# Kernel optimization log

Measured on AMD Instinct MI355X. Metric: run time of the kernel, lower is better.

The kernel has to match this reference:

```python
import jax, jax.numpy as jnp
import numpy as np
from jax import lax

NUM_HEADS = 8
HEAD_SIZE = 256  # hidden_size // num_heads

def _layernorm(x, g, b, eps=1e-5):
    mu = jnp.mean(x, axis=-1, keepdims=True)
    var = jnp.mean((x - mu) ** 2, axis=-1, keepdims=True)
    return (x - mu) * lax.rsqrt(var + eps) * g + b

def _groupnorm(x, g, b, num_groups, eps=1e-5):
    B, C = x.shape
    xr = x.reshape(B, num_groups, C // num_groups)
    mu = jnp.mean(xr, axis=-1, keepdims=True)
    var = jnp.mean((xr - mu) ** 2, axis=-1, keepdims=True)
    xn = ((xr - mu) * lax.rsqrt(var + eps)).reshape(B, C)
    return xn * g + b

def _block_diag(x, W, b):
    # x: (B, nb*fi), W: (nb, fi, fo), b: (nb, fo) -> (B, nb*fo)
    B = x.shape[0]
    nb, fi, fo = W.shape
    y = jnp.einsum('bnf,nfo->bno', x.reshape(B, nb, fi), W) + b
    return y.reshape(B, nb * fo)

def _causal_conv1d(x, w, b):
    # x: (B, L); w: (1,1,4). Pad-both-sides-3 then drop last 3 == left-pad 3.
    y = lax.conv_general_dilated(x[:, None, :], w, (1,), [(3, 0)])
    return y[:, 0, :] + b

def _mlstm_forward(x, ln_g, ln_b, Wupl, bupl, Wupr, bupr, conv_w, conv_b,
                   Wskip, bskip, Wq, bq, Wk, bk, Wv, bv, Wi, bi, Wf, bf,
                   Wo, bo, gn_g, gn_b, Wdown, bdown, c_prev, n_prev, m_prev):
    x_norm = _layernorm(x, ln_g, ln_b)
    x_up_left = x_norm @ Wupl + bupl           # (B, 2D)
    x_up_right = x_norm @ Wupr + bupr          # (B, H)
    x_conv = jax.nn.silu(_causal_conv1d(x_up_left, conv_w, conv_b))
    x_skip = x_conv @ Wskip + bskip            # (B, H)
    q = _block_diag(x_conv, Wq, bq)
    k = _block_diag(x_conv, Wk, bk) / (HEAD_SIZE ** 0.5)
    v = _block_diag(x_up_left, Wv, bv)
    i_tilde = x_conv @ Wi + bi
    f_tilde = x_conv @ Wf + bf
    o = jax.nn.sigmoid(x_up_left @ Wo + bo)
    m_t = jnp.maximum(f_tilde + m_prev, i_tilde)
    i_g = jnp.exp(i_tilde - m_t)
    f_g = jnp.exp(f_tilde + m_prev - m_t)
    c_t = f_g * c_prev + i_g * (v * k)
    n_t = f_g * n_prev + i_g * k
    denom = jnp.max(jnp.abs(n_t.T @ q), axis=1)  # (H,) broadcast over batch
    h_t = o * (c_t * q) / denom
    out = _groupnorm(h_t, gn_g, gn_b, NUM_HEADS) + x_skip
    out = out * jax.nn.silu(x_up_right)
    final = out @ Wdown + bdown + x
    return (final, h_t, c_t, n_t, m_t)

def setup_inputs():
    key = jax.random.key(0)
    ks = jax.random.split(key, 16)
    B, D, H, NB = 8192, 1024, 2048, 8
    UP = 2 * D
    rnd = lambda k, shp, s=0.02: jax.random.normal(k, shp, jnp.float32) * s
    return {
        'x': jax.random.normal(ks[0], (B, D), jnp.float32),
        'ln_g': jnp.ones((D,), jnp.float32), 'ln_b': jnp.zeros((D,), jnp.float32),
        'Wupl': rnd(ks[1], (D, UP)), 'bupl': jnp.zeros((UP,), jnp.float32),
        'Wupr': rnd(ks[2], (D, H)), 'bupr': jnp.zeros((H,), jnp.float32),
        'conv_w': rnd(ks[3], (1, 1, 4), 0.3), 'conv_b': jnp.zeros((1,), jnp.float32),
        'Wskip': rnd(ks[4], (UP, H)), 'bskip': jnp.zeros((H,), jnp.float32),
        'Wq': rnd(ks[5], (NB, UP // NB, H // NB)), 'bq': jnp.zeros((NB, H // NB), jnp.float32),
        'Wk': rnd(ks[6], (NB, UP // NB, H // NB)), 'bk': jnp.zeros((NB, H // NB), jnp.float32),
        'Wv': rnd(ks[7], (NB, UP // NB, H // NB)), 'bv': jnp.zeros((NB, H // NB), jnp.float32),
        'Wi': rnd(ks[8], (UP, H)), 'bi': jnp.zeros((H,), jnp.float32),
        'Wf': rnd(ks[9], (UP, H)), 'bf': jnp.zeros((H,), jnp.float32),
        'Wo': rnd(ks[10], (UP, H)), 'bo': jnp.zeros((H,), jnp.float32),
        'gn_g': jnp.ones((H,), jnp.float32), 'gn_b': jnp.zeros((H,), jnp.float32),
        'Wdown': rnd(ks[11], (H, D)), 'bdown': jnp.zeros((D,), jnp.float32),
        'c_prev': rnd(ks[12], (B, H)), 'n_prev': jnp.ones((B, H), jnp.float32),
        'm_prev': jnp.zeros((B, H), jnp.float32),
    }

def reference(x, ln_g, ln_b, Wupl, bupl, Wupr, bupr, conv_w, conv_b, Wskip, bskip,
              Wq, bq, Wk, bk, Wv, bv, Wi, bi, Wf, bf, Wo, bo, gn_g, gn_b,
              Wdown, bdown, c_prev, n_prev, m_prev):
    return _mlstm_forward(x, ln_g, ln_b, Wupl, bupl, Wupr, bupr, conv_w, conv_b,
                          Wskip, bskip, Wq, bq, Wk, bk, Wv, bv, Wi, bi, Wf, bf,
                          Wo, bo, gn_g, gn_b, Wdown, bdown, c_prev, n_prev, m_prev)
```

## Files before the change

### kernel.cpp

```cpp
#include <hip/hip_runtime.h>


typedef __bf16 bf16_t;
typedef bf16_t bf16x8 __attribute__((ext_vector_type(8)));
typedef bf16_t bf16x4 __attribute__((ext_vector_type(4)));
typedef float f32x4 __attribute__((ext_vector_type(4)));

#define B_ROWS 8192
#define DMODEL 1024
#define HDIM   2048

__device__ __forceinline__ void gload_lds16(const void* g, void* s) {
  __builtin_amdgcn_global_load_lds(
      (const __attribute__((address_space(1))) void*)g,
      (__attribute__((address_space(3))) void*)s, 16, 0, 0);
}

__device__ __forceinline__ float sigmoidf_(float x) { return 1.f / (1.f + __expf(-x)); }
__device__ __forceinline__ float siluf_(float x)    { return x / (1.f + __expf(-x)); }

__device__ __forceinline__ int xcd_swz(int lin, int nwg) {
  const int q = nwg >> 3, r = nwg & 7;
  const int xcd = lin & 7, sub = lin >> 3;
  return (xcd < r ? xcd * (q + 1) : r * (q + 1) + (xcd - r) * q) + sub;
}

__global__ __launch_bounds__(256) void wtrans_kernel(
    const float* __restrict__ in, bf16_t* __restrict__ out, int R, int C) {
  const int z = blockIdx.z;
  in  += (size_t)z * R * C;
  out += (size_t)z * R * C;
  __shared__ float tile[64][65];
  const int t = threadIdx.x;
  const int r0 = blockIdx.y * 64, c0 = blockIdx.x * 64;
#pragma unroll
  for (int j = 0; j < 4; ++j) {
    const int r = j * 16 + (t >> 4);
    const int c = (t & 15) * 4;
    float4 v = *(const float4*)&in[(size_t)(r0 + r) * C + c0 + c];
    tile[r][c] = v.x; tile[r][c + 1] = v.y; tile[r][c + 2] = v.z; tile[r][c + 3] = v.w;
  }
  __syncthreads();
#pragma unroll
  for (int j = 0; j < 2; ++j) {
    const int wi = j * 256 + t;
    const int oc = wi >> 3;
    const int orr = (wi & 7) * 8;
    bf16x8 v;
#pragma unroll
    for (int u = 0; u < 8; ++u) v[u] = (bf16_t)tile[orr + u][oc];
    *(bf16x8*)&out[(size_t)(c0 + oc) * R + r0 + orr] = v;
  }
}

__global__ __launch_bounds__(256) void ln_kernel(
    const float* __restrict__ x, const float* __restrict__ g,
    const float* __restrict__ b, bf16_t* __restrict__ out) {
  const int row = blockIdx.x;
  const int t = threadIdx.x;
  const float* xr = x + (size_t)row * DMODEL;
  float4 v = *(const float4*)&xr[t * 4];
  float s = v.x + v.y + v.z + v.w;
  float s2 = v.x * v.x + v.y * v.y + v.z * v.z + v.w * v.w;
#pragma unroll
  for (int off = 1; off < 64; off <<= 1) {
    s += __shfl_xor(s, off, 64);
    s2 += __shfl_xor(s2, off, 64);
  }
  __shared__ float ps[8];
  const int w = t >> 6;
  if ((t & 63) == 0) { ps[w] = s; ps[4 + w] = s2; }
  __syncthreads();
  s = ps[0] + ps[1] + ps[2] + ps[3];
  s2 = ps[4] + ps[5] + ps[6] + ps[7];
  const float mu = s / (float)DMODEL;
  const float var = s2 / (float)DMODEL - mu * mu;
  const float rstd = rsqrtf(var + 1e-5f);
  float4 gg = *(const float4*)&g[t * 4];
  float4 bb = *(const float4*)&b[t * 4];
  bf16x4 o;
  o[0] = (bf16_t)((v.x - mu) * rstd * gg.x + bb.x);
  o[1] = (bf16_t)((v.y - mu) * rstd * gg.y + bb.y);
  o[2] = (bf16_t)((v.z - mu) * rstd * gg.z + bb.z);
  o[3] = (bf16_t)((v.w - mu) * rstd * gg.w + bb.w);
  *(bf16x4*)&out[(size_t)row * DMODEL + t * 4] = o;
}

__global__ __launch_bounds__(256) void conv_kernel(
    const bf16_t* __restrict__ xin, const float* __restrict__ cw,
    const float* __restrict__ cb, bf16_t* __restrict__ yb) {
  const size_t idx = (size_t)blockIdx.x * blockDim.x + threadIdx.x;
  const int row = (int)(idx >> 9);
  const int c0 = ((int)idx & 511) * 4;
  const bf16_t* xr = xin + (size_t)row * HDIM;
  const float w0 = cw[0], w1 = cw[1], w2 = cw[2], w3 = cw[3], bb = cb[0];
  float xm3 = 0.f, xm2 = 0.f, xm1 = 0.f;
  if (c0 > 0) {
    bf16x4 p = *(const bf16x4*)&xr[c0 - 4];
    xm3 = (float)p[1]; xm2 = (float)p[2]; xm1 = (float)p[3];
  }
  bf16x4 xv4 = *(const bf16x4*)&xr[c0];
  float x0 = (float)xv4[0], x1 = (float)xv4[1], x2 = (float)xv4[2], x3 = (float)xv4[3];
  float y0 = w0 * xm3 + w1 * xm2 + w2 * xm1 + w3 * x0 + bb;
  float y1 = w0 * xm2 + w1 * xm1 + w2 * x0 + w3 * x1 + bb;
  float y2 = w0 * xm1 + w1 * x0 + w2 * x1 + w3 * x2 + bb;
  float y3 = w0 * x0 + w1 * x1 + w2 * x2 + w3 * x3 + bb;
  bf16x4 yb4;
  yb4[0] = (bf16_t)siluf_(y0); yb4[1] = (bf16_t)siluf_(y1);
  yb4[2] = (bf16_t)siluf_(y2); yb4[3] = (bf16_t)siluf_(y3);
  *(bf16x4*)&yb[(size_t)row * HDIM + c0] = yb4;
}

__global__ __launch_bounds__(256) void hgn_kernel(
    const bf16_t* __restrict__ o_pre, const float* __restrict__ q,
    const float* __restrict__ c_t, const float* __restrict__ denomf,
    const bf16_t* __restrict__ skip, const bf16_t* __restrict__ upr,
    const float* __restrict__ gn_g, const float* __restrict__ gn_b,
    float* __restrict__ h_out, bf16_t* __restrict__ act_out) {
  const int row = blockIdx.x;
  const int t = threadIdx.x;
  const size_t base = (size_t)row * HDIM + t * 8;
  const int i0 = t * 8;
  bf16x8 o8 = *(const bf16x8*)&o_pre[base];
  float h[8];
  float s = 0.f, s2 = 0.f;
#pragma unroll
  for (int j = 0; j < 2; ++j) {
    float4 qv = *(const float4*)&q[base + j * 4];
    float4 cv = *(const float4*)&c_t[base + j * 4];
#pragma unroll
    for (int u = 0; u < 4; ++u) {
      const int k = j * 4 + u;
      float hv = sigmoidf_((float)o8[k]) * ((const float*)&cv)[u] *
                 ((const float*)&qv)[u] / denomf[i0 + k];
      h[k] = hv;
      s += hv;
      s2 += hv * hv;
    }
  }
#pragma unroll
  for (int off = 1; off < 32; off <<= 1) {
    s += __shfl_xor(s, off, 64);
    s2 += __shfl_xor(s2, off, 64);
  }
  const float mu = s / 256.f;
  const float var = s2 / 256.f - mu * mu;
  const float rstd = rsqrtf(var + 1e-5f);
  float4 h0 = {h[0], h[1], h[2], h[3]};
  float4 h1 = {h[4], h[5], h[6], h[7]};
  *(float4*)&h_out[base] = h0;
  *(float4*)&h_out[base + 4] = h1;
  bf16x8 sk8 = *(const bf16x8*)&skip[base];
  bf16x8 up8 = *(const bf16x8*)&upr[base];
  bf16x8 a8;
#pragma unroll
  for (int j = 0; j < 2; ++j) {
    float4 gv = *(const float4*)&gn_g[i0 + j * 4];
    float4 bv = *(const float4*)&gn_b[i0 + j * 4];
#pragma unroll
    for (int u = 0; u < 4; ++u) {
      const int k = j * 4 + u;
      float y = (h[k] - mu) * rstd * ((const float*)&gv)[u] + ((const float*)&bv)[u];
      y = (y + (float)sk8[k]) * siluf_((float)up8[k]);
      a8[k] = (bf16_t)y;
    }
  }
  *(bf16x8*)&act_out[base] = a8;
}

template <int OUTMODE, bool RES>
__global__ __launch_bounds__(256) void gemm_kernel(
    const bf16_t* __restrict__ A, int lda, const bf16_t* __restrict__ Bt, int ldb,
    const float* __restrict__ bias, float* __restrict__ C, bf16_t* __restrict__ Cb,
    int ldc, const float* __restrict__ res, int ldres, int K, float scale,
    int zA, long long zB, int zBias, int zC) {
  const int z = blockIdx.z;
  A += (size_t)z * zA;
  Bt += (size_t)z * zB;
  if (bias) bias += (size_t)z * zBias;
  if (OUTMODE == 0) C += (size_t)z * zC; else Cb += (size_t)z * zC;
  const int brow = blockIdx.y * 128;
  const int bcol = blockIdx.x * 128;
  __shared__ bf16_t As[128 * 32];
  __shared__ bf16_t Bs[128 * 32];
  const int tid = threadIdx.x;
  const int w = tid >> 6, l = tid & 63;
  const int wr = w >> 1, wc = w & 1;
  const int lr = l & 15, kg = l >> 4;
  const int l4 = l & 3, ld4 = l >> 2;

  f32x4 acc[4][4];
  const f32x4 fzero = {0.f, 0.f, 0.f, 0.f};
#pragma unroll
  for (int m = 0; m < 4; ++m)
#pragma unroll
    for (int n = 0; n < 4; ++n) acc[m][n] = fzero;

  for (int kt = 0; kt < K; kt += 32) {
#pragma unroll
    for (int j = 0; j < 2; ++j) {
      const int rowX = w * 32 + j * 16 + ld4;
      gload_lds16(A + (size_t)(brow + rowX) * lda + kt + l4 * 8, &As[w * 1024 + j * 512]);
      gload_lds16(Bt + (size_t)(bcol + rowX) * ldb + kt + l4 * 8, &Bs[w * 1024 + j * 512]);
    }
    __syncthreads();
    bf16x8 a[4], b[4];
#pragma unroll
    for (int m = 0; m < 4; ++m)
      a[m] = *(const bf16x8*)&As[(wr * 64 + m * 16 + lr) * 32 + kg * 8];
#pragma unroll
    for (int n = 0; n < 4; ++n)
      b[n] = *(const bf16x8*)&Bs[(wc * 64 + n * 16 + lr) * 32 + kg * 8];
#pragma unroll
    for (int m = 0; m < 4; ++m)
#pragma unroll
      for (int n = 0; n < 4; ++n)
        acc[m][n] = __builtin_amdgcn_mfma_f32_16x16x32_bf16(a[m], b[n], acc[m][n], 0, 0, 0);
    __syncthreads();
  }

#pragma unroll
  for (int m = 0; m < 4; ++m) {
    const int row0 = brow + wr * 64 + m * 16 + kg * 4;
#pragma unroll
    for (int n = 0; n < 4; ++n) {
      const int col = bcol + wc * 64 + n * 16 + lr;
      const float bv = bias ? bias[col] : 0.f;
#pragma unroll
      for (int r = 0; r < 4; ++r) {
        const int row = row0 + r;
        float v = (acc[m][n][r] + bv) * scale;
        if (RES) v += res[(size_t)row * ldres + col];
        if (OUTMODE == 0) C[(size_t)row * ldc + col] = v;
        else Cb[(size_t)row * ldc + col] = (bf16_t)v;
      }
    }
  }
}

template <int OUTMODE , bool RES>
__global__ __launch_bounds__(512, 2) void gemm256_kernel(
    const bf16_t* __restrict__ A, int lda, const bf16_t* __restrict__ Bt, int ldb,
    const float* __restrict__ bias, float* __restrict__ C, bf16_t* __restrict__ Cb,
    int ldc, const float* __restrict__ res, int ldres, int K, float scale,
    long long zA, long long zB, long long zC) {
  const int z = blockIdx.z;
  A += (size_t)z * zA;
  Bt += (size_t)z * zB;
  if (OUTMODE == 0) C += (size_t)z * zC; else Cb += (size_t)z * zC;

  const int nwg = gridDim.x * gridDim.y;
  const int lin2 = xcd_swz(blockIdx.y * gridDim.x + blockIdx.x, nwg);
  const int bx = lin2 % gridDim.x, by = lin2 / gridDim.x;
  const int brow = by * 256, bcol = bx * 256;

  __shared__ bf16_t As[2][256 * 64];
  __shared__ bf16_t Bs[2][256 * 64];

  const int tid = threadIdx.x;
  const int l = tid & 63;
  const int w = tid >> 6;
  const int wr = w >> 2, wn = w & 3;
  const int lr = l & 15, kg = l >> 4;
  const int srow = tid >> 3;
  const int sslot = (tid & 7) ^ (srow & 7);

  f32x4 acc[8][4];
  const f32x4 fzero = {0.f, 0.f, 0.f, 0.f};
#pragma unroll
  for (int m = 0; m < 8; ++m)
#pragma unroll
    for (int n = 0; n < 4; ++n) acc[m][n] = fzero;

  const int NT = K >> 6;
  const bf16_t* Ag = A + (size_t)brow * lda;
  const bf16_t* Bg = Bt + (size_t)bcol * ldb;

  auto stage = [&](int t, int buf) {
    const size_t kof = (size_t)t * 64 + sslot * 8;
#pragma unroll
    for (int j = 0; j < 4; ++j) {
      const int r = j * 64 + srow;
      gload_lds16(Ag + (size_t)r * lda + kof, (char*)&As[buf][0] + (j * 512 + tid) * 16);
      gload_lds16(Bg + (size_t)r * ldb + kof, (char*)&Bs[buf][0] + (j * 512 + tid) * 16);
    }
  };

  stage(0, 0);
  stage(1, 1);

  for (int t = 0; t < NT; ++t) {
    if (t < NT - 1) asm volatile("s_waitcnt vmcnt(8)" ::: "memory");
    else            asm volatile("s_waitcnt vmcnt(0)" ::: "memory");
    __builtin_amdgcn_s_barrier();
    const int buf = t & 1;
#pragma unroll
    for (int kk = 0; kk < 2; ++kk) {
      bf16x8 a[8], b[4];
#pragma unroll
      for (int n = 0; n < 4; ++n) {
        const int r = wn * 64 + n * 16 + lr;
        b[n] = *(const bf16x8*)&Bs[buf][r * 64 + (((kk * 4 + kg) ^ (r & 7)) * 8)];
      }
#pragma unroll
      for (int m = 0; m < 8; ++m) {
        const int r = wr * 128 + m * 16 + lr;
        a[m] = *(const bf16x8*)&As[buf][r * 64 + (((kk * 4 + kg) ^ (r & 7)) * 8)];
      }
      __builtin_amdgcn_s_setprio(1);
#pragma unroll
      for (int m = 0; m < 8; ++m)
#pragma unroll
        for (int n = 0; n < 4; ++n)
          acc[m][n] = __builtin_amdgcn_mfma_f32_16x16x32_bf16(a[m], b[n], acc[m][n], 0, 0, 0);
      __builtin_amdgcn_s_setprio(0);
    }
    asm volatile("s_waitcnt lgkmcnt(0)" ::: "memory");
    __builtin_amdgcn_sched_barrier(0);
    __builtin_amdgcn_s_barrier();
    if (t + 2 < NT) stage(t + 2, buf);
  }

#pragma unroll
  for (int m = 0; m < 8; ++m) {
    const int row0 = brow + wr * 128 + m * 16 + kg * 4;
#pragma unroll
    for (int n = 0; n < 4; ++n) {
      const int col = bcol + wn * 64 + n * 16 + lr;
      const float bvv = bias ? bias[col] : 0.f;
#pragma unroll
      for (int r = 0; r < 4; ++r) {
        const int row = row0 + r;
        float v = (acc[m][n][r] + bvv) * scale;
        if (RES) v += res[(size_t)row * ldres + col];
        if (OUTMODE == 0) C[(size_t)row * ldc + col] = v;
        else Cb[(size_t)row * ldc + col] = (bf16_t)v;
      }
    }
  }
}

__global__ __launch_bounds__(512, 2) void ifgate256_kernel(
    const bf16_t* __restrict__ A,
    const bf16_t* __restrict__ Bi, const bf16_t* __restrict__ Bf,
    const float* __restrict__ bi, const float* __restrict__ bfv,
    const float* __restrict__ m_prev, const float* __restrict__ c_prev,
    const float* __restrict__ n_prev,
    const bf16_t* __restrict__ vb, const bf16_t* __restrict__ kb,
    float* __restrict__ m_out, float* __restrict__ c_out, float* __restrict__ n_out) {
  const int nwg = gridDim.x * gridDim.y;
  const int lin2 = xcd_swz(blockIdx.y * gridDim.x + blockIdx.x, nwg);
  const int bx = lin2 % gridDim.x, by = lin2 / gridDim.x;
  const int brow = by * 256, bcol = bx * 128;

  __shared__ bf16_t As[2][256 * 64];
  __shared__ bf16_t Bis[2][128 * 64];
  __shared__ bf16_t Bfs[2][128 * 64];

  const int tid = threadIdx.x;
  const int l = tid & 63;
  const int w = tid >> 6;
  const int wr = w >> 2, wn = w & 3;
  const int lr = l & 15, kg = l >> 4;
  const int srow = tid >> 3;
  const int sslot = (tid & 7) ^ (srow & 7);

  f32x4 acci[8][2], accf[8][2];
  const f32x4 fzero = {0.f, 0.f, 0.f, 0.f};
#pragma unroll
  for (int m = 0; m < 8; ++m)
#pragma unroll
    for (int n = 0; n < 2; ++n) { acci[m][n] = fzero; accf[m][n] = fzero; }

  const int NT = HDIM >> 6;
  const bf16_t* Ag = A + (size_t)brow * HDIM;
  const bf16_t* Big = Bi + (size_t)bcol * HDIM;
  const bf16_t* Bfg = Bf + (size_t)bcol * HDIM;

  auto stage = [&](int t, int buf) {
    const size_t kof = (size_t)t * 64 + sslot * 8;
#pragma unroll
    for (int j = 0; j < 4; ++j) {
      const int r = j * 64 + srow;
      gload_lds16(Ag + (size_t)r * HDIM + kof, (char*)&As[buf][0] + (j * 512 + tid) * 16);
    }
#pragma unroll
    for (int j = 0; j < 2; ++j) {
      const int r = j * 64 + srow;
      gload_lds16(Big + (size_t)r * HDIM + kof, (char*)&Bis[buf][0] + (j * 512 + tid) * 16);
      gload_lds16(Bfg + (size_t)r * HDIM + kof, (char*)&Bfs[buf][0] + (j * 512 + tid) * 16);
    }
  };

  stage(0, 0);
  stage(1, 1);

  for (int t = 0; t < NT; ++t) {
    if (t < NT - 1) asm volatile("s_waitcnt vmcnt(8)" ::: "memory");
    else            asm volatile("s_waitcnt vmcnt(0)" ::: "memory");
    __builtin_amdgcn_s_barrier();
    const int buf = t & 1;
#pragma unroll
    for (int kk = 0; kk < 2; ++kk) {
      bf16x8 a[8], b1[2], b2[2];
#pragma unroll
      for (int n = 0; n < 2; ++n) {
        const int r = wn * 32 + n * 16 + lr;
        const int eo = r * 64 + (((kk * 4 + kg) ^ (r & 7)) * 8);
        b1[n] = *(const bf16x8*)&Bis[buf][eo];
        b2[n] = *(const bf16x8*)&Bfs[buf][eo];
      }
#pragma unroll
      for (int m = 0; m < 8; ++m) {
        const int r = wr * 128 + m * 16 + lr;
        a[m] = *(const bf16x8*)&As[buf][r * 64 + (((kk * 4 + kg) ^ (r & 7)) * 8)];
      }
      __builtin_amdgcn_s_setprio(1);
#pragma unroll
      for (int m = 0; m < 8; ++m)
#pragma unroll
        for (int n = 0; n < 2; ++n) {
          acci[m][n] = __builtin_amdgcn_mfma_f32_16x16x32_bf16(a[m], b1[n], acci[m][n], 0, 0, 0);
          accf[m][n] = __builtin_amdgcn_mfma_f32_16x16x32_bf16(a[m], b2[n], accf[m][n], 0, 0, 0);
        }
      __builtin_amdgcn_s_setprio(0);
    }
    asm volatile("s_waitcnt lgkmcnt(0)" ::: "memory");
    __builtin_amdgcn_sched_barrier(0);
    __builtin_amdgcn_s_barrier();
    if (t + 2 < NT) stage(t + 2, buf);
  }

#pragma unroll
  for (int m = 0; m < 8; ++m) {
    const int row0 = brow + wr * 128 + m * 16 + kg * 4;
#pragma unroll
    for (int n = 0; n < 2; ++n) {
      const int col = bcol + wn * 32 + n * 16 + lr;
      const float biv = bi[col], bfvv = bfv[col];
#pragma unroll
      for (int r = 0; r < 4; ++r) {
        const int row = row0 + r;
        const size_t idx = (size_t)row * HDIM + col;
        const float it = acci[m][n][r] + biv;
        const float ft = accf[m][n][r] + bfvv;
        const float m1 = m_prev[idx];
        const float mt = fmaxf(ft + m1, it);
        const float ig = __expf(it - mt);
        const float fg = __expf(ft + m1 - mt);
        const float v1 = (float)vb[idx], k1 = (float)kb[idx];
        m_out[idx] = mt;
        c_out[idx] = fg * c_prev[idx] + ig * (v1 * k1);
        n_out[idx] = fg * n_prev[idx] + ig * k1;
      }
    }
  }
}

__global__ __launch_bounds__(256) void denom_reduce_kernel(
    const float* __restrict__ part, float* __restrict__ dmaxf) {
  const int i = blockIdx.x;
  const int t = threadIdx.x;
  float vmax = 0.f;
#pragma unroll
  for (int u = 0; u < 8; ++u) {
    const int j = u * 256 + t;
    float s = 0.f;
#pragma unroll
    for (int zz = 0; zz < 4; ++zz)
      s += part[(size_t)zz * HDIM * HDIM + (size_t)i * HDIM + j];
    vmax = fmaxf(vmax, fabsf(s));
  }
#pragma unroll
  for (int off = 1; off < 64; off <<= 1) vmax = fmaxf(vmax, __shfl_xor(vmax, off, 64));
  __shared__ float ps[4];
  if ((t & 63) == 0) ps[t >> 6] = vmax;
  __syncthreads();
  if (t == 0) dmaxf[i] = fmaxf(fmaxf(ps[0], ps[1]), fmaxf(ps[2], ps[3]));
}

extern "C" void kernel_launch(void* const* d_in, const int* in_sizes, int n_in,
                              void* d_out, int out_size, void* d_ws, size_t ws_size,
                              hipStream_t stream) {
  (void)in_sizes; (void)n_in; (void)out_size; (void)ws_size;
  const float* x      = (const float*)d_in[0];
  const float* ln_g   = (const float*)d_in[1];
  const float* ln_b   = (const float*)d_in[2];
  const float* Wupl   = (const float*)d_in[3];
  const float* bupl   = (const float*)d_in[4];
  const float* Wupr   = (const float*)d_in[5];
  const float* bupr   = (const float*)d_in[6];
  const float* conv_w = (const float*)d_in[7];
  const float* conv_b = (const float*)d_in[8];
  const float* Wskip  = (const float*)d_in[9];
  const float* bskip  = (const float*)d_in[10];
  const float* Wq     = (const float*)d_in[11];
  const float* bq     = (const float*)d_in[12];
  const float* Wk     = (const float*)d_in[13];
  const float* bk     = (const float*)d_in[14];
  const float* Wv     = (const float*)d_in[15];
  const float* bv     = (const float*)d_in[16];
  const float* Wi     = (const float*)d_in[17];
  const float* bi     = (const float*)d_in[18];
  const float* Wf     = (const float*)d_in[19];
  const float* bf_    = (const float*)d_in[20];
  const float* Wo     = (const float*)d_in[21];
  const float* bo     = (const float*)d_in[22];
  const float* gn_g   = (const float*)d_in[23];
  const float* gn_b   = (const float*)d_in[24];
  const float* Wdown  = (const float*)d_in[25];
  const float* bdown  = (const float*)d_in[26];
  const float* c_prev = (const float*)d_in[27];
  const float* n_prev = (const float*)d_in[28];
  const float* m_prev = (const float*)d_in[29];

  float* out_final = (float*)d_out;
  float* out_h = out_final + (size_t)B_ROWS * DMODEL;
  float* out_c = out_h + (size_t)B_ROWS * HDIM;
  float* out_n = out_c + (size_t)B_ROWS * HDIM;
  float* out_m = out_n + (size_t)B_ROWS * HDIM;

  char* ws = (char*)d_ws;
  size_t off = 0;
  auto alloc = [&](size_t bytes) -> void* {
    off = (off + 255) & ~(size_t)255;
    void* p = ws + off;
    off += bytes;
    return p;
  };
  const size_t BH = (size_t)B_ROWS * HDIM;
  const size_t BD = (size_t)B_ROWS * DMODEL;

  bf16_t* WuplT = (bf16_t*)alloc((size_t)DMODEL * HDIM * 2);
  bf16_t* WuprT = (bf16_t*)alloc((size_t)DMODEL * HDIM * 2);
  bf16_t* WskipT = (bf16_t*)alloc((size_t)HDIM * HDIM * 2);
  bf16_t* WiT = (bf16_t*)alloc((size_t)HDIM * HDIM * 2);
  bf16_t* WfT = (bf16_t*)alloc((size_t)HDIM * HDIM * 2);
  bf16_t* WoT = (bf16_t*)alloc((size_t)HDIM * HDIM * 2);
  bf16_t* WdownT = (bf16_t*)alloc((size_t)HDIM * DMODEL * 2);
  bf16_t* WqT = (bf16_t*)alloc((size_t)8 * 256 * 256 * 2);
  bf16_t* WkT = (bf16_t*)alloc((size_t)8 * 256 * 256 * 2);
  bf16_t* WvT = (bf16_t*)alloc((size_t)8 * 256 * 256 * 2);
  bf16_t* xnorm_b = (bf16_t*)alloc(BD * 2);
  bf16_t* xupl_b = (bf16_t*)alloc(BH * 2);
  bf16_t* xupr_b = (bf16_t*)alloc(BH * 2);
  bf16_t* xconv_b = (bf16_t*)alloc(BH * 2);
  bf16_t* xskip_b = (bf16_t*)alloc(BH * 2);
  bf16_t* o_b = (bf16_t*)alloc(BH * 2);
  float*  q_f = (float*)alloc(BH * 4);
  bf16_t* k_b = (bf16_t*)alloc(BH * 2);
  bf16_t* v_b = (bf16_t*)alloc(BH * 2);
  bf16_t* qT_b = (bf16_t*)alloc(BH * 2);
  bf16_t* nT_b = (bf16_t*)alloc(BH * 2);
  bf16_t* act_b = (bf16_t*)alloc(BH * 2);
  float*  part = (float*)alloc((size_t)4 * HDIM * HDIM * 4);
  float*  dmaxf = (float*)alloc(HDIM * 4);

  wtrans_kernel<<<dim3(HDIM / 64, DMODEL / 64, 1), 256, 0, stream>>>(Wupl, WuplT, DMODEL, HDIM);
  wtrans_kernel<<<dim3(HDIM / 64, DMODEL / 64, 1), 256, 0, stream>>>(Wupr, WuprT, DMODEL, HDIM);
  wtrans_kernel<<<dim3(HDIM / 64, HDIM / 64, 1), 256, 0, stream>>>(Wskip, WskipT, HDIM, HDIM);
  wtrans_kernel<<<dim3(HDIM / 64, HDIM / 64, 1), 256, 0, stream>>>(Wi, WiT, HDIM, HDIM);
  wtrans_kernel<<<dim3(HDIM / 64, HDIM / 64, 1), 256, 0, stream>>>(Wf, WfT, HDIM, HDIM);
  wtrans_kernel<<<dim3(HDIM / 64, HDIM / 64, 1), 256, 0, stream>>>(Wo, WoT, HDIM, HDIM);
  wtrans_kernel<<<dim3(DMODEL / 64, HDIM / 64, 1), 256, 0, stream>>>(Wdown, WdownT, HDIM, DMODEL);
  wtrans_kernel<<<dim3(4, 4, 8), 256, 0, stream>>>(Wq, WqT, 256, 256);
  wtrans_kernel<<<dim3(4, 4, 8), 256, 0, stream>>>(Wk, WkT, 256, 256);
  wtrans_kernel<<<dim3(4, 4, 8), 256, 0, stream>>>(Wv, WvT, 256, 256);

  ln_kernel<<<B_ROWS, 256, 0, stream>>>(x, ln_g, ln_b, xnorm_b);

  gemm256_kernel<2, false><<<dim3(HDIM / 256, B_ROWS / 256, 1), 512, 0, stream>>>(
      xnorm_b, DMODEL, WuplT, DMODEL, bupl, nullptr, xupl_b, HDIM, nullptr, 0,
      DMODEL, 1.f, 0, 0, 0);
  gemm256_kernel<2, false><<<dim3(HDIM / 256, B_ROWS / 256, 1), 512, 0, stream>>>(
      xnorm_b, DMODEL, WuprT, DMODEL, bupr, nullptr, xupr_b, HDIM, nullptr, 0,
      DMODEL, 1.f, 0, 0, 0);

  conv_kernel<<<(unsigned)(BH / 4 / 256), 256, 0, stream>>>(xupl_b, conv_w, conv_b, xconv_b);

  gemm256_kernel<2, false><<<dim3(HDIM / 256, B_ROWS / 256, 1), 512, 0, stream>>>(
      xconv_b, HDIM, WskipT, HDIM, bskip, nullptr, xskip_b, HDIM, nullptr, 0,
      HDIM, 1.f, 0, 0, 0);
  gemm256_kernel<2, false><<<dim3(HDIM / 256, B_ROWS / 256, 1), 512, 0, stream>>>(
      xupl_b, HDIM, WoT, HDIM, bo, nullptr, o_b, HDIM, nullptr, 0,
      HDIM, 1.f, 0, 0, 0);

  gemm_kernel<0, false><<<dim3(2, B_ROWS / 128, 8), 256, 0, stream>>>(
      xconv_b, HDIM, WqT, 256, bq, q_f, nullptr, HDIM, nullptr, 0,
      256, 1.f, 256, 256 * 256, 256, 256);
  gemm_kernel<2, false><<<dim3(2, B_ROWS / 128, 8), 256, 0, stream>>>(
      xconv_b, HDIM, WkT, 256, bk, nullptr, k_b, HDIM, nullptr, 0,
      256, 0.0625f, 256, 256 * 256, 256, 256);
  gemm_kernel<2, false><<<dim3(2, B_ROWS / 128, 8), 256, 0, stream>>>(
      xupl_b, HDIM, WvT, 256, bv, nullptr, v_b, HDIM, nullptr, 0,
      256, 1.f, 256, 256 * 256, 256, 256);

  ifgate256_kernel<<<dim3(HDIM / 128, B_ROWS / 256, 1), 512, 0, stream>>>(
      xconv_b, WiT, WfT, bi, bf_, m_prev, c_prev, n_prev, v_b, k_b,
      out_m, out_c, out_n);

  wtrans_kernel<<<dim3(HDIM / 64, B_ROWS / 64, 1), 256, 0, stream>>>(q_f, qT_b, B_ROWS, HDIM);
  wtrans_kernel<<<dim3(HDIM / 64, B_ROWS / 64, 1), 256, 0, stream>>>(out_n, nT_b, B_ROWS, HDIM);

  gemm256_kernel<0, false><<<dim3(HDIM / 256, HDIM / 256, 4), 512, 0, stream>>>(
      nT_b, B_ROWS, qT_b, B_ROWS, nullptr, part, nullptr, HDIM, nullptr, 0,
      2048, 1.f, 2048, 2048, (long long)HDIM * HDIM);
  denom_reduce_kernel<<<HDIM, 256, 0, stream>>>(part, dmaxf);

  hgn_kernel<<<B_ROWS, 256, 0, stream>>>(o_b, q_f, out_c, dmaxf, xskip_b,
                                         xupr_b, gn_g, gn_b, out_h, act_b);

  gemm256_kernel<0, true><<<dim3(DMODEL / 256, B_ROWS / 256, 1), 512, 0, stream>>>(
      act_b, HDIM, WdownT, HDIM, bdown, out_final, nullptr, DMODEL, x, DMODEL,
      HDIM, 1.f, 0, 0, 0);
}
```

Before: 1.351 ms.

## Switch GEMM kernels to 4-stage K=32 LDS ring with one barrier per step

Both the generic 256x256 GEMM and the fused i/f-gate GEMM now split K into 32-wide stages held in a 4-slot LDS ring, replacing 64-wide double buffering. Three stages are prefetched, and the next load is issued right after a single barrier instead of behind a second trailing barrier. The LDS swizzle is changed to match the 32-wide rows. The aim is deeper load/compute overlap and less barrier stall per MFMA batch. The cost is twice as many loop iterations and waitcnt points, with the same total LDS size.

```diff
diff --git a/kernel.cpp b/kernel.cpp
--- a/kernel.cpp
+++ b/kernel.cpp
@@ -254,16 +254,14 @@
   const int bx = lin2 % gridDim.x, by = lin2 / gridDim.x;
   const int brow = by * 256, bcol = bx * 256;
 
-  __shared__ bf16_t As[2][256 * 64];
-  __shared__ bf16_t Bs[2][256 * 64];
+  __shared__ bf16_t As[4][256 * 32];
+  __shared__ bf16_t Bs[4][256 * 32];
 
   const int tid = threadIdx.x;
   const int l = tid & 63;
   const int w = tid >> 6;
   const int wr = w >> 2, wn = w & 3;
   const int lr = l & 15, kg = l >> 4;
-  const int srow = tid >> 3;
-  const int sslot = (tid & 7) ^ (srow & 7);
 
   f32x4 acc[8][4];
   const f32x4 fzero = {0.f, 0.f, 0.f, 0.f};
@@ -272,53 +270,53 @@
 #pragma unroll
     for (int n = 0; n < 4; ++n) acc[m][n] = fzero;
 
-  const int NT = K >> 6;
+  const int NT2 = K >> 5;
   const bf16_t* Ag = A + (size_t)brow * lda;
   const bf16_t* Bg = Bt + (size_t)bcol * ldb;
 
-  auto stage = [&](int t, int buf) {
-    const size_t kof = (size_t)t * 64 + sslot * 8;
-#pragma unroll
-    for (int j = 0; j < 4; ++j) {
-      const int r = j * 64 + srow;
-      gload_lds16(Ag + (size_t)r * lda + kof, (char*)&As[buf][0] + (j * 512 + tid) * 16);
-      gload_lds16(Bg + (size_t)r * ldb + kof, (char*)&Bs[buf][0] + (j * 512 + tid) * 16);
+  auto stage = [&](int hh) {
+    const int slot = hh & 3;
+    const int kb = hh * 32;
+#pragma unroll
+    for (int j = 0; j < 2; ++j) {
+      const int L = j * 512 + tid;
+      const int row = L >> 2;
+      const int s = (L & 3) ^ ((L >> 3) & 3);
+      gload_lds16(Ag + (size_t)row * lda + kb + s * 8, (char*)&As[slot][0] + L * 16);
+      gload_lds16(Bg + (size_t)row * ldb + kb + s * 8, (char*)&Bs[slot][0] + L * 16);
     }
   };
 
-  stage(0, 0);
-  stage(1, 1);
-
-  for (int t = 0; t < NT; ++t) {
-    if (t < NT - 1) asm volatile("s_waitcnt vmcnt(8)" ::: "memory");
-    else            asm volatile("s_waitcnt vmcnt(0)" ::: "memory");
+  stage(0); stage(1); stage(2);
+
+  for (int h = 0; h < NT2; ++h) {
+    if (h >= NT2 - 1)      asm volatile("s_waitcnt vmcnt(0)" ::: "memory");
+    else if (h == NT2 - 2) asm volatile("s_waitcnt vmcnt(4)" ::: "memory");
+    else                   asm volatile("s_waitcnt vmcnt(8)" ::: "memory");
     __builtin_amdgcn_s_barrier();
-    const int buf = t & 1;
-#pragma unroll
-    for (int kk = 0; kk < 2; ++kk) {
-      bf16x8 a[8], b[4];
-#pragma unroll
-      for (int n = 0; n < 4; ++n) {
-        const int r = wn * 64 + n * 16 + lr;
-        b[n] = *(const bf16x8*)&Bs[buf][r * 64 + (((kk * 4 + kg) ^ (r & 7)) * 8)];
-      }
-#pragma unroll
-      for (int m = 0; m < 8; ++m) {
-        const int r = wr * 128 + m * 16 + lr;
-        a[m] = *(const bf16x8*)&As[buf][r * 64 + (((kk * 4 + kg) ^ (r & 7)) * 8)];
-      }
-      __builtin_amdgcn_s_setprio(1);
-#pragma unroll
-      for (int m = 0; m < 8; ++m)
-#pragma unroll
-        for (int n = 0; n < 4; ++n)
-          acc[m][n] = __builtin_amdgcn_mfma_f32_16x16x32_bf16(a[m], b[n], acc[m][n], 0, 0, 0);
-      __builtin_amdgcn_s_setprio(0);
+    __builtin_amdgcn_sched_barrier(0);
+    if (h + 3 < NT2) stage(h + 3);
+    const int buf = h & 3;
+    bf16x8 a[8], b[4];
+#pragma unroll
+    for (int n = 0; n < 4; ++n) {
+      const int r = wn * 64 + n * 16 + lr;
+      b[n] = *(const bf16x8*)&Bs[buf][r * 32 + ((kg ^ ((r >> 1) & 3)) * 8)];
+    }
+#pragma unroll
+    for (int m = 0; m < 8; ++m) {
+      const int r = wr * 128 + m * 16 + lr;
+      a[m] = *(const bf16x8*)&As[buf][r * 32 + ((kg ^ ((r >> 1) & 3)) * 8)];
     }
     asm volatile("s_waitcnt lgkmcnt(0)" ::: "memory");
     __builtin_amdgcn_sched_barrier(0);
-    __builtin_amdgcn_s_barrier();
-    if (t + 2 < NT) stage(t + 2, buf);
+    __builtin_amdgcn_s_setprio(1);
+#pragma unroll
+    for (int m = 0; m < 8; ++m)
+#pragma unroll
+      for (int n = 0; n < 4; ++n)
+        acc[m][n] = __builtin_amdgcn_mfma_f32_16x16x32_bf16(a[m], b[n], acc[m][n], 0, 0, 0);
+    __builtin_amdgcn_s_setprio(0);
   }
 
 #pragma unroll
@@ -353,17 +351,15 @@
   const int bx = lin2 % gridDim.x, by = lin2 / gridDim.x;
   const int brow = by * 256, bcol = bx * 128;
 
-  __shared__ bf16_t As[2][256 * 64];
-  __shared__ bf16_t Bis[2][128 * 64];
-  __shared__ bf16_t Bfs[2][128 * 64];
+  __shared__ bf16_t As[4][256 * 32];
+  __shared__ bf16_t Bis[4][128 * 32];
+  __shared__ bf16_t Bfs[4][128 * 32];
 
   const int tid = threadIdx.x;
   const int l = tid & 63;
   const int w = tid >> 6;
   const int wr = w >> 2, wn = w & 3;
   const int lr = l & 15, kg = l >> 4;
-  const int srow = tid >> 3;
-  const int sslot = (tid & 7) ^ (srow & 7);
 
   f32x4 acci[8][2], accf[8][2];
   const f32x4 fzero = {0.f, 0.f, 0.f, 0.f};
@@ -372,63 +368,64 @@
 #pragma unroll
     for (int n = 0; n < 2; ++n) { acci[m][n] = fzero; accf[m][n] = fzero; }
 
-  const int NT = HDIM >> 6;
+  const int NT2 = HDIM >> 5;
   const bf16_t* Ag = A + (size_t)brow * HDIM;
   const bf16_t* Big = Bi + (size_t)bcol * HDIM;
   const bf16_t* Bfg = Bf + (size_t)bcol * HDIM;
 
-  auto stage = [&](int t, int buf) {
-    const size_t kof = (size_t)t * 64 + sslot * 8;
-#pragma unroll
-    for (int j = 0; j < 4; ++j) {
-      const int r = j * 64 + srow;
-      gload_lds16(Ag + (size_t)r * HDIM + kof, (char*)&As[buf][0] + (j * 512 + tid) * 16);
-    }
+  auto stage = [&](int hh) {
+    const int slot = hh & 3;
+    const int kb2 = hh * 32;
 #pragma unroll
     for (int j = 0; j < 2; ++j) {
-      const int r = j * 64 + srow;
-      gload_lds16(Big + (size_t)r * HDIM + kof, (char*)&Bis[buf][0] + (j * 512 + tid) * 16);
-      gload_lds16(Bfg + (size_t)r * HDIM + kof, (char*)&Bfs[buf][0] + (j * 512 + tid) * 16);
+      const int L = j * 512 + tid;
+      const int row = L >> 2;
+      const int s = (L & 3) ^ ((L >> 3) & 3);
+      gload_lds16(Ag + (size_t)row * HDIM + kb2 + s * 8, (char*)&As[slot][0] + L * 16);
+    }
+    {
+      const int L = tid;
+      const int row = L >> 2;
+      const int s = (L & 3) ^ ((L >> 3) & 3);
+      gload_lds16(Big + (size_t)row * HDIM + kb2 + s * 8, (char*)&Bis[slot][0] + L * 16);
+      gload_lds16(Bfg + (size_t)row * HDIM + kb2 + s * 8, (char*)&Bfs[slot][0] + L * 16);
     }
   };
 
-  stage(0, 0);
-  stage(1, 1);
-
-  for (int t = 0; t < NT; ++t) {
-    if (t < NT - 1) asm volatile("s_waitcnt vmcnt(8)" ::: "memory");
-    else            asm volatile("s_waitcnt vmcnt(0)" ::: "memory");
+  stage(0); stage(1); stage(2);
+
+  for (int h = 0; h < NT2; ++h) {
+    if (h >= NT2 - 1)      asm volatile("s_waitcnt vmcnt(0)" ::: "memory");
+    else if (h == NT2 - 2) asm volatile("s_waitcnt vmcnt(4)" ::: "memory");
+    else                   asm volatile("s_waitcnt vmcnt(8)" ::: "memory");
     __builtin_amdgcn_s_barrier();
-    const int buf = t & 1;
-#pragma unroll
-    for (int kk = 0; kk < 2; ++kk) {
-      bf16x8 a[8], b1[2], b2[2];
-#pragma unroll
-      for (int n = 0; n < 2; ++n) {
-        const int r = wn * 32 + n * 16 + lr;
-        const int eo = r * 64 + (((kk * 4 + kg) ^ (r & 7)) * 8);
-        b1[n] = *(const bf16x8*)&Bis[buf][eo];
-        b2[n] = *(const bf16x8*)&Bfs[buf][eo];
-      }
-#pragma unroll
-      for (int m = 0; m < 8; ++m) {
-        const int r = wr * 128 + m * 16 + lr;
-        a[m] = *(const bf16x8*)&As[buf][r * 64 + (((kk * 4 + kg) ^ (r & 7)) * 8)];
-      }
-      __builtin_amdgcn_s_setprio(1);
-#pragma unroll
-      for (int m = 0; m < 8; ++m)
-#pragma unroll
-        for (int n = 0; n < 2; ++n) {
-          acci[m][n] = __builtin_amdgcn_mfma_f32_16x16x32_bf16(a[m], b1[n], acci[m][n], 0, 0, 0);
-          accf[m][n] = __builtin_amdgcn_mfma_f32_16x16x32_bf16(a[m], b2[n], accf[m][n], 0, 0, 0);
-        }
-      __builtin_amdgcn_s_setprio(0);
+    __builtin_amdgcn_sched_barrier(0);
+    if (h + 3 < NT2) stage(h + 3);
+    const int buf = h & 3;
+    bf16x8 a[8], b1[2], b2[2];
+#pragma unroll
+    for (int n = 0; n < 2; ++n) {
+      const int r = wn * 32 + n * 16 + lr;
+      const int eo = r * 32 + ((kg ^ ((r >> 1) & 3)) * 8);
+      b1[n] = *(const bf16x8*)&Bis[buf][eo];
+      b2[n] = *(const bf16x8*)&Bfs[buf][eo];
+    }
+#pragma unroll
+    for (int m = 0; m < 8; ++m) {
+      const int r = wr * 128 + m * 16 + lr;
+      a[m] = *(const bf16x8*)&As[buf][r * 32 + ((kg ^ ((r >> 1) & 3)) * 8)];
     }
     asm volatile("s_waitcnt lgkmcnt(0)" ::: "memory");
     __builtin_amdgcn_sched_barrier(0);
-    __builtin_amdgcn_s_barrier();
-    if (t + 2 < NT) stage(t + 2, buf);
+    __builtin_amdgcn_s_setprio(1);
+#pragma unroll
+    for (int m = 0; m < 8; ++m)
+#pragma unroll
+      for (int n = 0; n < 2; ++n) {
+        acci[m][n] = __builtin_amdgcn_mfma_f32_16x16x32_bf16(a[m], b1[n], acci[m][n], 0, 0, 0);
+        accf[m][n] = __builtin_amdgcn_mfma_f32_16x16x32_bf16(a[m], b2[n], accf[m][n], 0, 0, 0);
+      }
+    __builtin_amdgcn_s_setprio(0);
   }
 
 #pragma unroll
```

Result: slower. 1.460 ms (+8.0%).
